# Kernel tuning notes

Hardware: AMD Instinct MI355X
Metric: run time of the kernel (lower is better)

Reference implementation:

```python
import jax, jax.numpy as jnp
import numpy as np

N = 50000
E = 600000
D_IN = 128
D_OUT = 128
EPS = 1e-12  # F.normalize eps


def setup_inputs() -> dict:
    key = jax.random.key(0)
    ks = jax.random.split(key, 10)
    s = 1.0 / np.sqrt(D_IN)
    inp = {
        "x": jax.random.normal(ks[0], (N, D_IN), dtype=jnp.float32),
        "edge_index": jax.random.randint(ks[1], (2, E), 0, N, dtype=jnp.int64),
        # conv1: lin_l (with bias) applied to aggregated neighbors, lin_r (no bias) to root
        "W1l": jax.random.uniform(ks[2], (D_IN, D_IN), jnp.float32, -s, s),
        "b1": jax.random.uniform(ks[3], (D_IN,), jnp.float32, -s, s),
        "W1r": jax.random.uniform(ks[4], (D_IN, D_IN), jnp.float32, -s, s),
        # conv2
        "W2l": jax.random.uniform(ks[5], (D_IN, D_OUT), jnp.float32, -s, s),
        "b2": jax.random.uniform(ks[6], (D_OUT,), jnp.float32, -s, s),
        "W2r": jax.random.uniform(ks[7], (D_IN, D_OUT), jnp.float32, -s, s),
        # final fc
        "Wf": jax.random.uniform(ks[8], (D_OUT, D_OUT), jnp.float32, -s, s),
        "bf": jax.random.uniform(ks[9], (D_OUT,), jnp.float32, -s, s),
    }
    return inp


def _sage_conv(x, src, dst, Wl, bl, Wr):
    # mean-aggregate messages from source nodes onto destination nodes
    msgs = x[src]  # [E, d] gather
    agg = jax.ops.segment_sum(msgs, dst, num_segments=N)  # [N, d]
    cnt = jax.ops.segment_sum(jnp.ones((src.shape[0],), x.dtype), dst, num_segments=N)
    agg = agg / jnp.maximum(cnt, 1.0)[:, None]  # isolated nodes -> 0
    out = agg @ Wl + bl + x @ Wr
    # L2 normalize per node (PyG normalize=True)
    nrm = jnp.sqrt(jnp.sum(out * out, axis=-1, keepdims=True))
    return out / jnp.maximum(nrm, EPS)


def reference(x, edge_index, W1l, b1, W1r, W2l, b2, W2r, Wf, bf):
    src, dst = edge_index[0], edge_index[1]
    h = jax.nn.relu(_sage_conv(x, src, dst, W1l, b1, W1r))
    h = jax.nn.relu(_sage_conv(h, src, dst, W2l, b2, W2r))
    return h @ Wf + bf
```

## Files before the change

### kernel.cpp

```cpp
#include <hip/hip_runtime.h>
#include <hip/hip_fp16.h>

#define D 128
#define SCAN_B 256

typedef __attribute__((ext_vector_type(8))) short bf16x8;
typedef __attribute__((ext_vector_type(4))) float f32x4;

__device__ __forceinline__ unsigned short f2bf(float f) {
    unsigned u = __float_as_uint(f);
    unsigned r = u + 0x7FFFu + ((u >> 16) & 1u);
    return (unsigned short)(r >> 16);
}
__device__ __forceinline__ float bf2f(unsigned short h) {
    return __uint_as_float(((unsigned)h) << 16);
}

__global__ void count_kernel(const int* __restrict__ ei, int E, int* __restrict__ cnt) {
    int t = blockIdx.x * blockDim.x + threadIdx.x;
    if (t < E) atomicAdd(&cnt[ei[E + t]], 1);
}

__global__ void scan_pass1(const int* __restrict__ cnt, int* __restrict__ rs,
                           int* __restrict__ bsum, int N) {
    __shared__ int lds[SCAN_B];
    int tid = threadIdx.x;
    int i = blockIdx.x * SCAN_B + tid;
    int v = (i < N) ? cnt[i] : 0;
    lds[tid] = v;
    __syncthreads();
    for (int o = 1; o < SCAN_B; o <<= 1) {
        int t = (tid >= o) ? lds[tid - o] : 0;
        __syncthreads();
        lds[tid] += t;
        __syncthreads();
    }
    if (i < N) rs[i] = lds[tid] - v;
    if (tid == SCAN_B - 1) bsum[blockIdx.x] = lds[tid];
}

__global__ void scan_pass2(int* __restrict__ bsum, int nb) {
    __shared__ int lds[SCAN_B];
    int tid = threadIdx.x;
    int v = (tid < nb) ? bsum[tid] : 0;
    lds[tid] = v;
    __syncthreads();
    for (int o = 1; o < SCAN_B; o <<= 1) {
        int t = (tid >= o) ? lds[tid - o] : 0;
        __syncthreads();
        lds[tid] += t;
        __syncthreads();
    }
    if (tid < nb) bsum[tid] = lds[tid] - v;
}

__global__ void scan_pass3(int* __restrict__ rs, int* __restrict__ cursor,
                           const int* __restrict__ bsum, const int* __restrict__ cnt,
                           float* __restrict__ inv, int N) {
    int i = blockIdx.x * SCAN_B + threadIdx.x;
    if (i < N) {
        int v = rs[i] + bsum[blockIdx.x];
        rs[i] = v;
        cursor[i] = v;
        inv[i] = 1.0f / (float)max(cnt[i], 1);
    }
}

__global__ void fill_kernel(const int* __restrict__ ei, int E,
                            int* __restrict__ cursor, int* __restrict__ csr) {
    int e = blockIdx.x * blockDim.x + threadIdx.x;
    if (e < E) {
        int src = ei[e], dst = ei[E + e];
        int pos = atomicAdd(&cursor[dst], 1);
        csr[pos] = src;
    }
}

__global__ void cvt_half_kernel(const float* __restrict__ x, __half* __restrict__ xh, int n8) {
    int i = blockIdx.x * blockDim.x + threadIdx.x;
    if (i >= n8) return;
    const float4* x4 = (const float4*)x;
    float4 a = x4[2 * i], b = x4[2 * i + 1];
    __half2 h0 = __floats2half2_rn(a.x, a.y);
    __half2 h1 = __floats2half2_rn(a.z, a.w);
    __half2 h2 = __floats2half2_rn(b.x, b.y);
    __half2 h3 = __floats2half2_rn(b.z, b.w);
    uint4 o;
    o.x = *(const unsigned*)&h0;
    o.y = *(const unsigned*)&h1;
    o.z = *(const unsigned*)&h2;
    o.w = *(const unsigned*)&h3;
    ((uint4*)xh)[i] = o;
}

__device__ __forceinline__ void acc8(uint4 v, float* s) {
    const __half2* h = reinterpret_cast<const __half2*>(&v);
    float2 f0 = __half22float2(h[0]);
    float2 f1 = __half22float2(h[1]);
    float2 f2 = __half22float2(h[2]);
    float2 f3 = __half22float2(h[3]);
    s[0] += f0.x; s[1] += f0.y; s[2] += f1.x; s[3] += f1.y;
    s[4] += f2.x; s[5] += f2.y; s[6] += f3.x; s[7] += f3.y;
}

__global__ void aggregate_kernel(const __half* __restrict__ xh, const int* __restrict__ csr,
                                 const int* __restrict__ rs, const int* __restrict__ cnt,
                                 const float* __restrict__ inv, float* __restrict__ agg,
                                 int N) {
    int t = blockIdx.x * blockDim.x + threadIdx.x;
    int node = t >> 4;
    int c = t & 15;
    if (node >= N) return;
    int deg = cnt[node];
    int st = rs[node];
    const uint4* x4 = (const uint4*)xh;
    float s[8] = {0.f, 0.f, 0.f, 0.f, 0.f, 0.f, 0.f, 0.f};
    int i = 0;
    for (; i + 4 <= deg; i += 4) {
        int n0 = csr[st + i + 0], n1 = csr[st + i + 1];
        int n2 = csr[st + i + 2], n3 = csr[st + i + 3];
        uint4 v0 = x4[(size_t)n0 * 16 + c];
        uint4 v1 = x4[(size_t)n1 * 16 + c];
        uint4 v2 = x4[(size_t)n2 * 16 + c];
        uint4 v3 = x4[(size_t)n3 * 16 + c];
        acc8(v0, s); acc8(v1, s); acc8(v2, s); acc8(v3, s);
    }
    for (; i < deg; i++) {
        int n0 = csr[st + i];
        uint4 v0 = x4[(size_t)n0 * 16 + c];
        acc8(v0, s);
    }
    float iv = inv[node];
    float* dst = agg + (size_t)node * D + c * 8;
    ((float4*)dst)[0] = make_float4(s[0] * iv, s[1] * iv, s[2] * iv, s[3] * iv);
    ((float4*)dst)[1] = make_float4(s[4] * iv, s[5] * iv, s[6] * iv, s[7] * iv);
}

__global__ void pack_kernel(const float* __restrict__ W1l, const float* __restrict__ W1r,
                            const float* __restrict__ W2l, const float* __restrict__ W2r,
                            const float* __restrict__ Wf, unsigned short* __restrict__ pw) {
    int idx = blockIdx.x * blockDim.x + threadIdx.x;
    if (idx >= 5 * 2048) return;
    int w = idx >> 11;
    int r = idx & 2047;
    int ks = r >> 9;
    int t = (r >> 6) & 7;
    int lane = r & 63;
    int q = lane >> 4, n = lane & 15;
    const float* W = (w == 0) ? W1l : (w == 1) ? W1r : (w == 2) ? W2l : (w == 3) ? W2r : Wf;
    unsigned short* dh = pw + (size_t)w * 32768;
    unsigned short* dl = dh + 16384;
    int off = ((ks * 8 + t) * 64 + lane) * 8;
#pragma unroll
    for (int j = 0; j < 8; j++) {
        float v = W[(size_t)(ks * 32 + q * 8 + j) * D + t * 16 + n];
        unsigned short hb = f2bf(v);
        dh[off + j] = hb;
        dl[off + j] = f2bf(v - bf2f(hb));
    }
}

__device__ __forceinline__ void split8(const float* av, bf16x8& hi, bf16x8& lo) {
#pragma unroll
    for (int j = 0; j < 8; j++) {
        unsigned short hb = f2bf(av[j]);
        hi[j] = (short)hb;
        lo[j] = (short)f2bf(av[j] - bf2f(hb));
    }
}

template <int FUSE_FC>
__global__ __launch_bounds__(256) void mfma_gemm(
        const float* __restrict__ Aagg, const float* __restrict__ Ax,
        const unsigned short* __restrict__ W0h, const unsigned short* __restrict__ W0lo,
        const unsigned short* __restrict__ W1h, const unsigned short* __restrict__ W1lo,
        const float* __restrict__ bias,
        const unsigned short* __restrict__ Wfh, const unsigned short* __restrict__ Wflo,
        const float* __restrict__ bfin,
        float* __restrict__ out, __half* __restrict__ outh, int N) {
    __shared__ unsigned short Hs[FUSE_FC ? 4 * 4096 : 4];

    const int tid = threadIdx.x;
    const int lane = tid & 63;
    const int wave = tid >> 6;
    const int c = lane & 15;
    const int q = lane >> 4;
    const int R = blockIdx.x * 64 + wave * 16;

    int row0 = R + c;
    if (row0 >= N) row0 = N - 1;
    const size_t a_base = (size_t)row0 * D;

    f32x4 acc[8];
#pragma unroll
    for (int t = 0; t < 8; t++)
#pragma unroll
        for (int r = 0; r < 4; r++) acc[t][r] = 0.0f;

#pragma unroll
    for (int ks = 0; ks < 8; ks++) {
        const float* Asrc = (ks < 4) ? Aagg : Ax;
        const int kl = ks & 3;
        const int koff = kl * 32 + q * 8;
        float av[8];
        *((float4*)&av[0]) = *((const float4*)(Asrc + a_base + koff));
        *((float4*)&av[4]) = *((const float4*)(Asrc + a_base + koff + 4));
        bf16x8 ah, al;
        split8(av, ah, al);

        const uint4* Wh4 = (const uint4*)((ks < 4) ? W0h : W1h);
        const uint4* Wl4 = (const uint4*)((ks < 4) ? W0lo : W1lo);
#pragma unroll
        for (int t = 0; t < 8; t++) {
            int fi = (kl * 8 + t) * 64 + lane;
            bf16x8 bh = __builtin_bit_cast(bf16x8, Wh4[fi]);
            bf16x8 blo = __builtin_bit_cast(bf16x8, Wl4[fi]);
            acc[t] = __builtin_amdgcn_mfma_f32_16x16x32_bf16(ah, bh, acc[t], 0, 0, 0);
            acc[t] = __builtin_amdgcn_mfma_f32_16x16x32_bf16(al, bh, acc[t], 0, 0, 0);
            acc[t] = __builtin_amdgcn_mfma_f32_16x16x32_bf16(ah, blo, acc[t], 0, 0, 0);
        }
    }

#pragma unroll
    for (int t = 0; t < 8; t++) {
        float bv = bias[t * 16 + c];
#pragma unroll
        for (int r = 0; r < 4; r++) acc[t][r] += bv;
    }
#pragma unroll
    for (int r = 0; r < 4; r++) {
        float v = 0.0f;
#pragma unroll
        for (int t = 0; t < 8; t++) v += acc[t][r] * acc[t][r];
        v += __shfl_xor(v, 1, 16);
        v += __shfl_xor(v, 2, 16);
        v += __shfl_xor(v, 4, 16);
        v += __shfl_xor(v, 8, 16);
        float rn = 1.0f / fmaxf(sqrtf(v), 1e-12f);
#pragma unroll
        for (int t = 0; t < 8; t++) acc[t][r] = fmaxf(acc[t][r] * rn, 0.0f);
    }

    if (!FUSE_FC) {
#pragma unroll
        for (int t = 0; t < 8; t++)
#pragma unroll
            for (int r = 0; r < 4; r++) {
                int row = R + q * 4 + r;
                if (row < N) {
                    float v = acc[t][r];
                    out[(size_t)row * D + t * 16 + c] = v;
                    if (outh) outh[(size_t)row * D + t * 16 + c] = __float2half_rn(v);
                }
            }
        return;
    }

    unsigned short* Hw = &Hs[wave * 4096];
#pragma unroll
    for (int t = 0; t < 8; t++)
#pragma unroll
        for (int r = 0; r < 4; r++) {
            int row = q * 4 + r;
            int col = t * 16 + c;
            int ks2 = col >> 5, c32 = col & 31;
            int off = ((ks2 * 64) + (c32 >> 3) * 16 + row) * 8 + (c32 & 7);
            float hv = acc[t][r];
            unsigned short hb = f2bf(hv);
            Hw[off] = hb;
            Hw[2048 + off] = f2bf(hv - bf2f(hb));
        }

    f32x4 acc2[8];
#pragma unroll
    for (int t = 0; t < 8; t++) {
        float bv = bfin[t * 16 + c];
#pragma unroll
        for (int r = 0; r < 4; r++) acc2[t][r] = bv;
    }
    const uint4* Wfh4 = (const uint4*)Wfh;
    const uint4* Wfl4 = (const uint4*)Wflo;
#pragma unroll
    for (int ks2 = 0; ks2 < 4; ks2++) {
        bf16x8 ah2 = __builtin_bit_cast(bf16x8, ((const uint4*)Hw)[ks2 * 64 + lane]);
        bf16x8 al2 = __builtin_bit_cast(bf16x8, ((const uint4*)(Hw + 2048))[ks2 * 64 + lane]);
#pragma unroll
        for (int t = 0; t < 8; t++) {
            int fi = (ks2 * 8 + t) * 64 + lane;
            bf16x8 bh = __builtin_bit_cast(bf16x8, Wfh4[fi]);
            bf16x8 blo = __builtin_bit_cast(bf16x8, Wfl4[fi]);
            acc2[t] = __builtin_amdgcn_mfma_f32_16x16x32_bf16(ah2, bh, acc2[t], 0, 0, 0);
            acc2[t] = __builtin_amdgcn_mfma_f32_16x16x32_bf16(al2, bh, acc2[t], 0, 0, 0);
            acc2[t] = __builtin_amdgcn_mfma_f32_16x16x32_bf16(ah2, blo, acc2[t], 0, 0, 0);
        }
    }

#pragma unroll
    for (int t = 0; t < 8; t++)
#pragma unroll
        for (int r = 0; r < 4; r++) {
            int row = R + q * 4 + r;
            if (row < N) out[(size_t)row * D + t * 16 + c] = acc2[t][r];
        }
}

extern "C" void kernel_launch(void* const* d_in, const int* in_sizes, int n_in,
                              void* d_out, int out_size, void* d_ws, size_t ws_size,
                              hipStream_t stream) {
    const float* x   = (const float*)d_in[0];
    const int*   ei  = (const int*)d_in[1];
    const float* W1l = (const float*)d_in[2];
    const float* b1  = (const float*)d_in[3];
    const float* W1r = (const float*)d_in[4];
    const float* W2l = (const float*)d_in[5];
    const float* b2  = (const float*)d_in[6];
    const float* W2r = (const float*)d_in[7];
    const float* Wf  = (const float*)d_in[8];
    const float* bf  = (const float*)d_in[9];
    float* out = (float*)d_out;

    int N = in_sizes[0] / D;
    int E = in_sizes[1] / 2;

    float* ws     = (float*)d_ws;
    float* agg    = ws;
    float* inv    = ws + (size_t)N * D;
    int*   rs     = (int*)(inv + N);
    int*   cnt    = rs + N;
    int*   cursor = cnt + N;
    int*   bsum   = cursor + N;
    int*   csr    = bsum + 256;
    unsigned short* pw = (unsigned short*)(csr + E);
    unsigned short* pW1lh = pw + 0 * 32768, *pW1ll = pW1lh + 16384;
    unsigned short* pW1rh = pw + 1 * 32768, *pW1rl = pW1rh + 16384;
    unsigned short* pW2lh = pw + 2 * 32768, *pW2ll = pW2lh + 16384;
    unsigned short* pW2rh = pw + 3 * 32768, *pW2rl = pW2rh + 16384;
    unsigned short* pWfh  = pw + 4 * 32768, *pWfl  = pWfh + 16384;
    __half* hb = (__half*)(pw + 5 * 32768);

    int nb = (N + SCAN_B - 1) / SCAN_B;

    hipMemsetAsync(cnt, 0, (size_t)N * sizeof(int), stream);
    pack_kernel<<<40, 256, 0, stream>>>(W1l, W1r, W2l, W2r, Wf, pw);
    int n8 = N * 16;
    cvt_half_kernel<<<(n8 + 255) / 256, 256, 0, stream>>>(x, hb, n8);
    count_kernel<<<(E + 255) / 256, 256, 0, stream>>>(ei, E, cnt);
    scan_pass1<<<nb, SCAN_B, 0, stream>>>(cnt, rs, bsum, N);
    scan_pass2<<<1, SCAN_B, 0, stream>>>(bsum, nb);
    scan_pass3<<<nb, SCAN_B, 0, stream>>>(rs, cursor, bsum, cnt, inv, N);
    fill_kernel<<<(E + 255) / 256, 256, 0, stream>>>(ei, E, cursor, csr);

    int agg_blocks = (N * 16 + 255) / 256;
    int gemm_blocks = (N + 63) / 64;

    aggregate_kernel<<<agg_blocks, 256, 0, stream>>>(hb, csr, rs, cnt, inv, agg, N);
    mfma_gemm<0><<<gemm_blocks, 256, 0, stream>>>(agg, x, pW1lh, pW1ll, pW1rh, pW1rl, b1,
                                                  nullptr, nullptr, nullptr, out, hb, N);

    aggregate_kernel<<<agg_blocks, 256, 0, stream>>>(hb, csr, rs, cnt, inv, agg, N);
    mfma_gemm<1><<<gemm_blocks, 256, 0, stream>>>(agg, out, pW2lh, pW2ll, pW2rh, pW2rl, b2,
                                                  pWfh, pWfl, bf, out, nullptr, N);
}
```

Before: 307.9 us.

## Split GEMM output columns across wave pairs with shared-memory norm reduction

Each block now covers 32 rows rather than 64, and two waves share each 16-row group, each computing half of the 128 output columns. The per-row L2 norm partial sums are combined through shared memory behind a barrier, and the fused FC input tile is rebuilt in a padded row-major LDS layout that both column halves read. This doubles the number of blocks and halves the accumulator registers per wave, which should raise occupancy and parallelism. In exchange, each wave pair loads the A rows twice and the kernel gains block-wide syncs.

```diff
diff --git a/kernel.cpp b/kernel.cpp
--- a/kernel.cpp
+++ b/kernel.cpp
@@ -3,6 +3,7 @@
 
 #define D 128
 #define SCAN_B 256
+#define HLD 136
 
 typedef __attribute__((ext_vector_type(8))) short bf16x8;
 typedef __attribute__((ext_vector_type(4))) float f32x4;
@@ -178,22 +179,25 @@
         const unsigned short* __restrict__ Wfh, const unsigned short* __restrict__ Wflo,
         const float* __restrict__ bfin,
         float* __restrict__ out, __half* __restrict__ outh, int N) {
-    __shared__ unsigned short Hs[FUSE_FC ? 4 * 4096 : 4];
+    __shared__ float normbuf[2][2][16];
+    __shared__ unsigned short Hs[FUSE_FC ? 2 * 2 * 16 * HLD : 4];
 
     const int tid = threadIdx.x;
     const int lane = tid & 63;
     const int wave = tid >> 6;
+    const int rg = wave >> 1;
+    const int cg = wave & 1;
     const int c = lane & 15;
     const int q = lane >> 4;
-    const int R = blockIdx.x * 64 + wave * 16;
+    const int R = blockIdx.x * 32 + rg * 16;
 
     int row0 = R + c;
     if (row0 >= N) row0 = N - 1;
     const size_t a_base = (size_t)row0 * D;
 
-    f32x4 acc[8];
-#pragma unroll
-    for (int t = 0; t < 8; t++)
+    f32x4 acc[4];
+#pragma unroll
+    for (int t = 0; t < 4; t++)
 #pragma unroll
         for (int r = 0; r < 4; r++) acc[t][r] = 0.0f;
 
@@ -211,8 +215,8 @@
         const uint4* Wh4 = (const uint4*)((ks < 4) ? W0h : W1h);
         const uint4* Wl4 = (const uint4*)((ks < 4) ? W0lo : W1lo);
 #pragma unroll
-        for (int t = 0; t < 8; t++) {
-            int fi = (kl * 8 + t) * 64 + lane;
+        for (int t = 0; t < 4; t++) {
+            int fi = (kl * 8 + cg * 4 + t) * 64 + lane;
             bf16x8 bh = __builtin_bit_cast(bf16x8, Wh4[fi]);
             bf16x8 blo = __builtin_bit_cast(bf16x8, Wl4[fi]);
             acc[t] = __builtin_amdgcn_mfma_f32_16x16x32_bf16(ah, bh, acc[t], 0, 0, 0);
@@ -222,59 +226,72 @@
     }
 
 #pragma unroll
-    for (int t = 0; t < 8; t++) {
-        float bv = bias[t * 16 + c];
+    for (int t = 0; t < 4; t++) {
+        float bv = bias[(cg * 4 + t) * 16 + c];
 #pragma unroll
         for (int r = 0; r < 4; r++) acc[t][r] += bv;
     }
+    float vr[4];
 #pragma unroll
     for (int r = 0; r < 4; r++) {
         float v = 0.0f;
 #pragma unroll
-        for (int t = 0; t < 8; t++) v += acc[t][r] * acc[t][r];
+        for (int t = 0; t < 4; t++) v += acc[t][r] * acc[t][r];
         v += __shfl_xor(v, 1, 16);
         v += __shfl_xor(v, 2, 16);
         v += __shfl_xor(v, 4, 16);
         v += __shfl_xor(v, 8, 16);
-        float rn = 1.0f / fmaxf(sqrtf(v), 1e-12f);
-#pragma unroll
-        for (int t = 0; t < 8; t++) acc[t][r] = fmaxf(acc[t][r] * rn, 0.0f);
+        vr[r] = v;
+    }
+    if (c == 0) {
+#pragma unroll
+        for (int r = 0; r < 4; r++) normbuf[rg][cg][q * 4 + r] = vr[r];
+    }
+    __syncthreads();
+#pragma unroll
+    for (int r = 0; r < 4; r++) {
+        int row = q * 4 + r;
+        float tot = normbuf[rg][0][row] + normbuf[rg][1][row];
+        float rn = 1.0f / fmaxf(sqrtf(tot), 1e-12f);
+#pragma unroll
+        for (int t = 0; t < 4; t++) acc[t][r] = fmaxf(acc[t][r] * rn, 0.0f);
     }
 
     if (!FUSE_FC) {
 #pragma unroll
-        for (int t = 0; t < 8; t++)
+        for (int t = 0; t < 4; t++)
 #pragma unroll
             for (int r = 0; r < 4; r++) {
                 int row = R + q * 4 + r;
                 if (row < N) {
                     float v = acc[t][r];
-                    out[(size_t)row * D + t * 16 + c] = v;
-                    if (outh) outh[(size_t)row * D + t * 16 + c] = __float2half_rn(v);
+                    size_t idx = (size_t)row * D + (cg * 4 + t) * 16 + c;
+                    out[idx] = v;
+                    if (outh) outh[idx] = __float2half_rn(v);
                 }
             }
         return;
     }
 
-    unsigned short* Hw = &Hs[wave * 4096];
-#pragma unroll
-    for (int t = 0; t < 8; t++)
+    unsigned short* Hhi = &Hs[rg * 2 * 16 * HLD];
+    unsigned short* Hlo = Hhi + 16 * HLD;
+#pragma unroll
+    for (int t = 0; t < 4; t++)
 #pragma unroll
         for (int r = 0; r < 4; r++) {
             int row = q * 4 + r;
-            int col = t * 16 + c;
-            int ks2 = col >> 5, c32 = col & 31;
-            int off = ((ks2 * 64) + (c32 >> 3) * 16 + row) * 8 + (c32 & 7);
+            int col = (cg * 4 + t) * 16 + c;
             float hv = acc[t][r];
             unsigned short hb = f2bf(hv);
-            Hw[off] = hb;
-            Hw[2048 + off] = f2bf(hv - bf2f(hb));
+            Hhi[row * HLD + col] = hb;
+            Hlo[row * HLD + col] = f2bf(hv - bf2f(hb));
         }
-
-    f32x4 acc2[8];
-#pragma unroll
-    for (int t = 0; t < 8; t++) {
-        float bv = bfin[t * 16 + c];
+    __syncthreads();
+
+    f32x4 acc2[4];
+#pragma unroll
+    for (int t = 0; t < 4; t++) {
+        float bv = bfin[(cg * 4 + t) * 16 + c];
 #pragma unroll
         for (int r = 0; r < 4; r++) acc2[t][r] = bv;
     }
@@ -282,11 +299,11 @@
     const uint4* Wfl4 = (const uint4*)Wflo;
 #pragma unroll
     for (int ks2 = 0; ks2 < 4; ks2++) {
-        bf16x8 ah2 = __builtin_bit_cast(bf16x8, ((const uint4*)Hw)[ks2 * 64 + lane]);
-        bf16x8 al2 = __builtin_bit_cast(bf16x8, ((const uint4*)(Hw + 2048))[ks2 * 64 + lane]);
-#pragma unroll
-        for (int t = 0; t < 8; t++) {
-            int fi = (ks2 * 8 + t) * 64 + lane;
+        bf16x8 ah2 = __builtin_bit_cast(bf16x8, *(const uint4*)&Hhi[c * HLD + ks2 * 32 + q * 8]);
+        bf16x8 al2 = __builtin_bit_cast(bf16x8, *(const uint4*)&Hlo[c * HLD + ks2 * 32 + q * 8]);
+#pragma unroll
+        for (int t = 0; t < 4; t++) {
+            int fi = (ks2 * 8 + cg * 4 + t) * 64 + lane;
             bf16x8 bh = __builtin_bit_cast(bf16x8, Wfh4[fi]);
             bf16x8 blo = __builtin_bit_cast(bf16x8, Wfl4[fi]);
             acc2[t] = __builtin_amdgcn_mfma_f32_16x16x32_bf16(ah2, bh, acc2[t], 0, 0, 0);
@@ -296,11 +313,11 @@
     }
 
 #pragma unroll
-    for (int t = 0; t < 8; t++)
+    for (int t = 0; t < 4; t++)
 #pragma unroll
         for (int r = 0; r < 4; r++) {
             int row = R + q * 4 + r;
-            if (row < N) out[(size_t)row * D + t * 16 + c] = acc2[t][r];
+            if (row < N) out[(size_t)row * D + (cg * 4 + t) * 16 + c] = acc2[t][r];
         }
 }
 
@@ -351,7 +368,7 @@
     fill_kernel<<<(E + 255) / 256, 256, 0, stream>>>(ei, E, cursor, csr);
 
     int agg_blocks = (N * 16 + 255) / 256;
-    int gemm_blocks = (N + 63) / 64;
+    int gemm_blocks = (N + 31) / 32;
 
     aggregate_kernel<<<agg_blocks, 256, 0, stream>>>(hb, csr, rs, cnt, inv, agg, N);
     mfma_gemm<0><<<gemm_blocks, 256, 0, stream>>>(agg, x, pW1lh, pW1ll, pW1rh, pW1rl, b1,
```

After: 289.5 us. 1.06x faster.
